# Kernel optimization log

Hardware: AMD Instinct MI355X
Metric: run time of the kernel (lower is better)

## Reference

```python
import jax, jax.numpy as jnp
import numpy as np

TOTAL_WORDS = 10000
EMBED_LEN = 100
SEQ_LEN = 80
BATCH = 2048
UNITS = 1024


def setup_inputs() -> dict:
    key = jax.random.key(0)
    ks = jax.random.split(key, 8)
    inputs = jax.random.randint(ks[0], (BATCH, SEQ_LEN), 0, TOTAL_WORDS)
    s = 0.02
    emb = jax.random.normal(ks[1], (TOTAL_WORDS, EMBED_LEN), jnp.float32) * s
    W0 = jax.random.normal(ks[2], (EMBED_LEN, 4 * UNITS), jnp.float32) * s
    U0 = jax.random.normal(ks[3], (UNITS, 4 * UNITS), jnp.float32) * s
    b0 = jnp.zeros((4 * UNITS,), jnp.float32)
    W1 = jax.random.normal(ks[4], (UNITS, 4 * UNITS), jnp.float32) * s
    U1 = jax.random.normal(ks[5], (UNITS, 4 * UNITS), jnp.float32) * s
    b1 = jnp.zeros((4 * UNITS,), jnp.float32)
    fcW = jax.random.normal(ks[6], (UNITS, 1), jnp.float32) * s
    fcb = jnp.zeros((1,), jnp.float32)
    return {"inputs": inputs, "emb": emb, "W0": W0, "U0": U0, "b0": b0,
            "W1": W1, "U1": U1, "b1": b1, "fcW": fcW, "fcb": fcb}


def _lstm_step(x, h, c, W, U, b):
    # Keras LSTMCell gate order: i, f, g(candidate), o
    z = x @ W + h @ U + b  # [B, 4*units]
    i, f, g, o = jnp.split(z, 4, axis=-1)
    i = jax.nn.sigmoid(i)
    f = jax.nn.sigmoid(f)
    g = jnp.tanh(g)
    o = jax.nn.sigmoid(o)
    c_new = f * c + i * g
    h_new = o * jnp.tanh(c_new)
    return h_new, c_new


def reference(inputs, emb, W0, U0, b0, W1, U1, b1, fcW, fcb):
    x = emb[inputs]                      # [B, T, E]
    xs = jnp.transpose(x, (1, 0, 2))     # [T, B, E] for scan over time
    B = inputs.shape[0]
    U = U0.shape[0]
    init = (jnp.zeros((B, U), x.dtype), jnp.zeros((B, U), x.dtype),
            jnp.zeros((B, U), x.dtype), jnp.zeros((B, U), x.dtype))

    def step(carry, xt):
        h0, c0, h1, c1 = carry
        h0, c0 = _lstm_step(xt, h0, c0, W0, U0, b0)
        h1, c1 = _lstm_step(h0, h1, c1, W1, U1, b1)
        return (h0, c0, h1, c1), None

    (h0, c0, h1, c1), _ = jax.lax.scan(step, init, xs)
    logits = h1 @ fcW + fcb              # [B, 1]
    return jax.nn.sigmoid(logits)
```

## Files before the change

### kernel.cpp

```cpp
#include <hip/hip_runtime.h>

#define DEVI __device__ __forceinline__

typedef __attribute__((ext_vector_type(4))) float f4;
typedef long long i64t;

DEVI unsigned char f2fp8(float x) {
  int p = __builtin_amdgcn_cvt_pk_fp8_f32(x, x, 0, false);
  return (unsigned char)(p & 0xff);
}
DEVI float fp82f(unsigned char b) {
  return __builtin_amdgcn_cvt_f32_fp8((int)b, 0);
}
DEVI float sigmoidf_(float x) { return 1.f / (1.f + __expf(-x)); }
DEVI float tanhf_(float x) {
  float ax = fabsf(x);
  float e = __expf(-2.f * ax);
  float t = (1.f - e) / (1.f + e);
  return x < 0.f ? -t : t;
}

#define GLDS16(g, l) __builtin_amdgcn_global_load_lds( \
    (const __attribute__((address_space(1))) void*)(g), \
    (__attribute__((address_space(3))) void*)(l), 16, 0, 0)

#define SCALE_UP 64.0f
#define SCALE_DN (1.0f / 4096.0f)


__global__ void k_conv_emb(const float* __restrict__ emb, unsigned char* __restrict__ ep) {
  int i = blockIdx.x * 256 + threadIdx.x;
  if (i >= 10000 * 128) return;
  int r = i >> 7, c = i & 127;
  ep[i] = (c < 100) ? f2fp8(emb[r * 100 + c] * SCALE_UP) : (unsigned char)0;
}

DEVI int permn(int n) {
  int g = n >> 10, u = n & 1023;
  return (u >> 5) * 128 + ((u >> 4) & 1) * 64 + g * 16 + (u & 15);
}
DEVI int kswz(int klog, int row) {
  return (klog & ~63) | (((((klog >> 3) & 7) ^ ((row >> 1) & 7))) << 3) | (klog & 7);
}

__global__ void k_conv_w0(const float* __restrict__ W0, const float* __restrict__ U0,
                          unsigned char* __restrict__ WT) {
  int i = blockIdx.x * 256 + threadIdx.x;
  if (i >= 4096 * 1152) return;
  int n = i / 1152, k = i - n * 1152;
  float v;
  if (k < 100) v = W0[k * 4096 + n];
  else if (k < 128) v = 0.f;
  else v = U0[(k - 128) * 4096 + n];
  int np = permn(n);
  WT[(size_t)np * 1152 + kswz(k, np)] = f2fp8(v * SCALE_UP);
}

__global__ void k_conv_w1(const float* __restrict__ W1, const float* __restrict__ U1,
                          unsigned char* __restrict__ WT) {
  int i = blockIdx.x * 256 + threadIdx.x;
  if (i >= 4096 * 2048) return;
  int n = i >> 11, k = i & 2047;
  float v = (k < 1024) ? W1[k * 4096 + n] : U1[(k - 1024) * 4096 + n];
  int np = permn(n);
  WT[(size_t)np * 2048 + kswz(k, np)] = f2fp8(v * SCALE_UP);
}


template<int K1, int KTOT, bool GATHER>
DEVI void lstm_phase(int m0, int n0, char* smem,
    const unsigned char* __restrict__ src1,
    const unsigned char* __restrict__ src2,
    const int* __restrict__ idx, int t,
    const unsigned char* __restrict__ WT,
    const float* __restrict__ bias,
    float* __restrict__ cbuf,
    unsigned char* __restrict__ hout)
{
  const int tid = threadIdx.x;

  const int lr = tid >> 2;
  const int c16 = (tid & 3) * 16;
  const int csw = (((tid & 3) ^ ((tid >> 3) & 3))) * 16;

  const unsigned char* g1 = nullptr;
  if (GATHER) {
    int w = idx[(m0 + lr) * 80 + t];
    g1 = src1 + (size_t)w * K1 + csw;
  }

  const unsigned char* wbase = WT + (size_t)(n0 + lr) * KTOT + c16;
  const unsigned char* a1b = src1 + (size_t)(m0 + lr) * 1024 + c16;
  const unsigned char* a2b = src2 + (size_t)(m0 + lr) * 1024 + c16 - K1;

  char* const LA0 = smem;
  char* const LB0 = smem + 8192;
  char* const LA1 = smem + 16384;
  char* const LB1 = smem + 24576;

  auto stage = [&](int kb, char* la, char* lb) {
    const int kc = kb * 64;
    if (GATHER && kc < K1) {
      GLDS16(g1 + kc, la + tid * 16);
    } else {
      const unsigned char* g = (!GATHER && kc < K1) ? a1b + kc : a2b + kc;
      GLDS16(g, la + tid * 16);
    }
    GLDS16(wbase + kc, lb + tid * 16);
  };

  const int lane = tid & 63;
  const int wv = tid >> 6;
  const int wm = wv >> 1;
  const int wn = wv & 1;
  const int cl = lane & 15;
  const int qd = lane >> 4;
  const int qh = qd >> 1, qb = qd & 1;
  const int g8s = (cl >> 1) & 7;
  const int ko8_0 = ((0 + qd) ^ g8s) << 3;
  const int ko8_1 = ((4 + qd) ^ g8s) << 3;
  const int g4s = (cl >> 1) & 3;
  const int ko16_0 = ((qh ^ g4s) << 4) + qb * 8;
  const int ko16_1 = (((2 + qh) ^ g4s) << 4) + qb * 8;

  f4 acc[2][4];
  const f4 fz = {0.f, 0.f, 0.f, 0.f};
#pragma unroll
  for (int a = 0; a < 2; ++a)
#pragma unroll
    for (int b = 0; b < 4; ++b) acc[a][b] = fz;

  auto compute = [&](char* la, char* lb, int koA0, int koA1) {
#pragma unroll
    for (int kk = 0; kk < 2; ++kk) {
      const int koA = kk ? koA1 : koA0;
      const int koB = kk ? ko8_1 : ko8_0;
      i64t af[2], bfr[4];
#pragma unroll
      for (int mi = 0; mi < 2; ++mi)
        af[mi] = *(const i64t*)(la + (wm * 32 + mi * 16 + cl) * 64 + koA);
#pragma unroll
      for (int j = 0; j < 4; ++j)
        bfr[j] = *(const i64t*)(lb + (wn * 64 + j * 16 + cl) * 64 + koB);
#pragma unroll
      for (int mi = 0; mi < 2; ++mi)
#pragma unroll
        for (int j = 0; j < 4; ++j)
          acc[mi][j] = __builtin_amdgcn_mfma_f32_16x16x32_fp8_fp8(
              af[mi], bfr[j], acc[mi][j], 0, 0, 0);
    }
  };

  stage(0, LA0, LB0);

  constexpr int NKB = KTOT / 64;
  static_assert(NKB % 2 == 0, "K-loop unroll-2 requires even NKB");
#pragma unroll 1
  for (int kbp = 0; kbp < NKB / 2; ++kbp) {
    const int kb0 = kbp * 2;
    __syncthreads();
    stage(kb0 + 1, LA1, LB1);
    {
      const bool A16 = GATHER && (kb0 * 64) < K1;
      compute(LA0, LB0, A16 ? ko16_0 : ko8_0, A16 ? ko16_1 : ko8_1);
    }
    __syncthreads();
    if (kb0 + 2 < NKB) stage(kb0 + 2, LA0, LB0);
    {
      const bool A16 = GATHER && ((kb0 + 1) * 64) < K1;
      compute(LA1, LB1, A16 ? ko16_0 : ko8_0, A16 ? ko16_1 : ko8_1);
    }
  }

  const int u = n0 / 4 + wn * 16 + cl;
  const int uhi = u & ~63;
  const int uc8 = (u >> 3) & 7;
  const int ulo = u & 7;
  const float bi = bias[u];
  const float bff = bias[1024 + u];
  const float bg = bias[2048 + u];
  const float bo = bias[3072 + u];
#pragma unroll
  for (int mi = 0; mi < 2; ++mi) {
    int mbase = m0 + wm * 32 + mi * 16 + qd * 4;
#pragma unroll
    for (int r = 0; r < 4; ++r) {
      int m = mbase + r;
      int fm = (qd * 2 + (r >> 1)) & 7;
      int hcol = uhi | ((uc8 ^ fm) << 3) | ulo;
      float gi = sigmoidf_(acc[mi][0][r] * SCALE_DN + bi);
      float gf = sigmoidf_(acc[mi][1][r] * SCALE_DN + bff);
      float gg = tanhf_(acc[mi][2][r] * SCALE_DN + bg);
      float go = sigmoidf_(acc[mi][3][r] * SCALE_DN + bo);
      size_t coff = (size_t)m * 1024 + u;
      float cn = gf * cbuf[coff] + gi * gg;
      cbuf[coff] = cn;
      hout[(size_t)m * 1024 + hcol] = f2fp8(go * tanhf_(cn) * SCALE_UP);
    }
  }
}

__global__ __launch_bounds__(512, 4) void k_step(
    int mode,
    const unsigned char* embp, const unsigned char* h0in,
    const int* idx, int t,
    const unsigned char* WT0, const float* b0, float* c0, unsigned char* h0out,
    const unsigned char* h0prev, const unsigned char* h1in,
    const unsigned char* WT1, const float* b1, float* c1, unsigned char* h1out)
{
  extern __shared__ char smem[];
  const int blk = blockIdx.x;
  const int m0 = (blk >> 5) * 128;
  const int n0 = (blk & 31) * 128;
  if (mode != 2)
    lstm_phase<128, 1152, true>(m0, n0, smem, embp, h0in, idx, t,
                                WT0, b0, c0, h0out);
  if (mode != 0)
    lstm_phase<1024, 2048, false>(m0, n0, smem, h0prev, h1in, nullptr, 0,
                                  WT1, b1, c1, h1out);
}


__global__ void k_fc(const unsigned char* __restrict__ h1,
                     const float* __restrict__ fcW, const float* __restrict__ fcb,
                     float* __restrict__ out) {
  int wv = threadIdx.x >> 6;
  int lane = threadIdx.x & 63;
  int row = blockIdx.x * 4 + wv;
  if (row >= 2048) return;
  const unsigned char* hr = h1 + (size_t)row * 1024;
  const int f = (row >> 1) & 7;
  float s = 0.f;
  for (int k = lane; k < 1024; k += 64) {
    int ks = (k & ~63) | ((((k >> 3) & 7) ^ f) << 3) | (k & 7);
    s += fp82f(hr[ks]) * fcW[k];
  }
#pragma unroll
  for (int off = 32; off > 0; off >>= 1) s += __shfl_down(s, off);
  if (lane == 0) out[row] = sigmoidf_(s * (1.0f / SCALE_UP) + fcb[0]);
}


extern "C" void kernel_launch(void* const* d_in, const int* in_sizes, int n_in,
                              void* d_out, int out_size, void* d_ws, size_t ws_size,
                              hipStream_t stream) {
  const int*   idx = (const int*)d_in[0];
  const float* emb = (const float*)d_in[1];
  const float* W0  = (const float*)d_in[2];
  const float* U0  = (const float*)d_in[3];
  const float* b0  = (const float*)d_in[4];
  const float* W1  = (const float*)d_in[5];
  const float* U1  = (const float*)d_in[6];
  const float* b1  = (const float*)d_in[7];
  const float* fcW = (const float*)d_in[8];
  const float* fcb = (const float*)d_in[9];
  float* out = (float*)d_out;

  char* ws = (char*)d_ws;
  unsigned char* embp = (unsigned char*)(ws);
  unsigned char* WT0  = (unsigned char*)(ws + 1280000);
  unsigned char* WT1  = (unsigned char*)(ws + 5998592);
  unsigned char* h0b[2] = {(unsigned char*)(ws + 14387200),
                           (unsigned char*)(ws + 16484352)};
  unsigned char* h1b[2] = {(unsigned char*)(ws + 18581504),
                           (unsigned char*)(ws + 20678656)};
  float* c0 = (float*)(ws + 22775808);
  float* c1 = (float*)(ws + 31164416);

  hipMemsetAsync(ws + 14387200, 0, 25165824, stream);

  k_conv_emb<<<5000, 256, 0, stream>>>(emb, embp);
  k_conv_w0<<<18432, 256, 0, stream>>>(W0, U0, WT0);
  k_conv_w1<<<32768, 256, 0, stream>>>(W1, U1, WT1);

  k_step<<<512, 512, 32768, stream>>>(0, embp, h0b[1], idx, 0,
                                      WT0, b0, c0, h0b[0],
                                      nullptr, nullptr, WT1, b1, c1, nullptr);
  for (int t = 1; t < 80; ++t) {
    k_step<<<512, 512, 32768, stream>>>(1, embp, h0b[(t + 1) & 1], idx, t,
                                        WT0, b0, c0, h0b[t & 1],
                                        h0b[(t - 1) & 1], h1b[t & 1],
                                        WT1, b1, c1, h1b[(t + 1) & 1]);
  }
  k_step<<<512, 512, 32768, stream>>>(2, nullptr, nullptr, nullptr, 0,
                                      WT0, b0, c0, nullptr,
                                      h0b[1], h1b[0], WT1, b1, c1, h1b[1]);

  k_fc<<<512, 256, 0, stream>>>(h1b[1], fcW, fcb, out);
}
```

Before: 3.914 ms.

## Deepen K-loop pipeline to four LDS stages with explicit vmcnt waits

Replaces the two-buffer double-buffered K loop with a four-slot ring that keeps three tile loads in flight, using explicit s_waitcnt vmcnt counts and a raw barrier in place of __syncthreads. The aim is to hide global-to-LDS load latency for the small per-step GEMMs. The loop is now fully unrolled, LDS per block doubles to 64KB, and a barrier is added between the two phases. The larger LDS footprint may reduce how many blocks fit per CU.

```diff
diff --git a/kernel.cpp b/kernel.cpp
--- a/kernel.cpp
+++ b/kernel.cpp
@@ -93,12 +93,10 @@
   const unsigned char* a1b = src1 + (size_t)(m0 + lr) * 1024 + c16;
   const unsigned char* a2b = src2 + (size_t)(m0 + lr) * 1024 + c16 - K1;
 
-  char* const LA0 = smem;
-  char* const LB0 = smem + 8192;
-  char* const LA1 = smem + 16384;
-  char* const LB1 = smem + 24576;
-
-  auto stage = [&](int kb, char* la, char* lb) {
+  char* const SAs[4] = {smem, smem + 16384, smem + 32768, smem + 49152};
+
+  auto stage = [&](int kb, char* la) {
+    char* lb = la + 8192;
     const int kc = kb * 64;
     if (GATHER && kc < K1) {
       GLDS16(g1 + kc, la + tid * 16);
@@ -130,7 +128,8 @@
 #pragma unroll
     for (int b = 0; b < 4; ++b) acc[a][b] = fz;
 
-  auto compute = [&](char* la, char* lb, int koA0, int koA1) {
+  auto compute = [&](char* la, int koA0, int koA1) {
+    char* lb = la + 8192;
 #pragma unroll
     for (int kk = 0; kk < 2; ++kk) {
       const int koA = kk ? koA1 : koA0;
@@ -151,25 +150,23 @@
     }
   };
 
-  stage(0, LA0, LB0);
+  stage(0, SAs[0]);
+  stage(1, SAs[1]);
+  stage(2, SAs[2]);
 
   constexpr int NKB = KTOT / 64;
-  static_assert(NKB % 2 == 0, "K-loop unroll-2 requires even NKB");
-#pragma unroll 1
-  for (int kbp = 0; kbp < NKB / 2; ++kbp) {
-    const int kb0 = kbp * 2;
-    __syncthreads();
-    stage(kb0 + 1, LA1, LB1);
-    {
-      const bool A16 = GATHER && (kb0 * 64) < K1;
-      compute(LA0, LB0, A16 ? ko16_0 : ko8_0, A16 ? ko16_1 : ko8_1);
-    }
-    __syncthreads();
-    if (kb0 + 2 < NKB) stage(kb0 + 2, LA0, LB0);
-    {
-      const bool A16 = GATHER && ((kb0 + 1) * 64) < K1;
-      compute(LA1, LB1, A16 ? ko16_0 : ko8_0, A16 ? ko16_1 : ko8_1);
-    }
+#pragma unroll
+  for (int kb = 0; kb < NKB; ++kb) {
+    if (kb < NKB - 2)
+      asm volatile("s_waitcnt vmcnt(4)" ::: "memory");
+    else if (kb == NKB - 2)
+      asm volatile("s_waitcnt vmcnt(2)" ::: "memory");
+    else
+      asm volatile("s_waitcnt vmcnt(0)" ::: "memory");
+    __builtin_amdgcn_s_barrier();
+    if (kb + 3 < NKB) stage(kb + 3, SAs[(kb + 3) & 3]);
+    const bool A16 = GATHER && (kb * 64) < K1;
+    compute(SAs[kb & 3], A16 ? ko16_0 : ko8_0, A16 ? ko16_1 : ko8_1);
   }
 
   const int u = n0 / 4 + wn * 16 + cl;
@@ -215,6 +212,8 @@
   if (mode != 2)
     lstm_phase<128, 1152, true>(m0, n0, smem, embp, h0in, idx, t,
                                 WT0, b0, c0, h0out);
+  if (mode == 1)
+    __syncthreads();
   if (mode != 0)
     lstm_phase<1024, 2048, false>(m0, n0, smem, h0prev, h1in, nullptr, 0,
                                   WT1, b1, c1, h1out);
@@ -273,16 +272,16 @@
   k_conv_w0<<<18432, 256, 0, stream>>>(W0, U0, WT0);
   k_conv_w1<<<32768, 256, 0, stream>>>(W1, U1, WT1);
 
-  k_step<<<512, 512, 32768, stream>>>(0, embp, h0b[1], idx, 0,
+  k_step<<<512, 512, 65536, stream>>>(0, embp, h0b[1], idx, 0,
                                       WT0, b0, c0, h0b[0],
                                       nullptr, nullptr, WT1, b1, c1, nullptr);
   for (int t = 1; t < 80; ++t) {
-    k_step<<<512, 512, 32768, stream>>>(1, embp, h0b[(t + 1) & 1], idx, t,
+    k_step<<<512, 512, 65536, stream>>>(1, embp, h0b[(t + 1) & 1], idx, t,
                                         WT0, b0, c0, h0b[t & 1],
                                         h0b[(t - 1) & 1], h1b[t & 1],
                                         WT1, b1, c1, h1b[(t + 1) & 1]);
   }
-  k_step<<<512, 512, 32768, stream>>>(2, nullptr, nullptr, nullptr, 0,
+  k_step<<<512, 512, 65536, stream>>>(2, nullptr, nullptr, nullptr, 0,
                                       WT0, b0, c0, nullptr,
                                       h0b[1], h1b[0], WT1, b1, c1, h1b[1]);
 
```

Result: faster. 3.797 ms (-3.0%).
